# Optimization experiments

Hardware: AMD Instinct MI355X
Metric: run time of the kernel (lower is better)

Reference implementation:

```python
import jax, jax.numpy as jnp
import numpy as np
from jax import lax

BETA = 1.0
EPS_BIS = 0.1   # eps_threshold of FIND_MIN
N_ITER = 24     # enough bisection steps for any interval width seen here
N_BOX = 2097152
TINY = 1e-12


def _slog(x):
    return jnp.log(jnp.maximum(x, TINY))


def _sl1(x):  # smooth_l1_loss
    d = jnp.abs(x)
    return jnp.where(d < BETA, 0.5 * d * d / BETA, d - 0.5 * BETA)


def _sl1p(x):  # smooth_l1_loss_prime
    return jnp.clip(x / BETA, -1.0, 1.0)


def _xi_prime(w, wp, wh):
    return 0.5 * _sl1p(0.5 * (w - wh)) + _sl1p(_slog(w) - _slog(wp)) / jnp.maximum(w, TINY)


def _sigma(w, wp, wh):
    return w * _xi_prime(w, wp, wh)


def _xi(w, wp, wh):  # bbox_loss at x=(w-wh)/2
    return _sl1(0.5 * (w - wh)) + _sl1(_slog(wp) - _slog(w))


def _bisect(u, v, f):
    # vectorized FIND_MIN: early-exit endpoints + bisection to width < EPS_BIS
    fu, fv = f(u), f(v)

    def body(i, c):
        lo, hi = c
        act = (hi - lo) >= EPS_BIS
        m = 0.5 * (lo + hi)
        pos = f(m) >= 0
        lo = jnp.where(act & ~pos, m, lo)
        hi = jnp.where(act & pos, m, hi)
        return lo, hi

    lo, hi = lax.fori_loop(0, N_ITER, body, (u, v))
    m = 0.5 * (lo + hi)
    return jnp.where(fu >= 0, u, jnp.where(fv <= 0, v, m))


def _solve_o1(wp, wh, a1, b1):
    w0 = b1 - a1
    fxp = lambda w: _xi_prime(w, wp, wh)
    fsg = lambda w: _sigma(w, wp, wh)
    # branch A: max(w0, wh) < wp
    rA = _bisect(jnp.maximum(w0, wh), wp, fxp)
    eb = np.float32(np.exp(BETA))
    emin = np.float32(np.exp(min(BETA, 1.0)))
    e1 = np.float32(np.e)
    base = jnp.maximum(w0, jnp.maximum(wh - 2.0 * BETA, e1 * wp))
    disc = jnp.sqrt(jnp.maximum(1.0 - 32.0 / jnp.maximum(wh * wh, TINY), 0.0))
    r1 = _bisect(jnp.maximum(w0, wp), jnp.minimum(emin * wp, wh), fxp)                 # J1
    r2 = _bisect(jnp.maximum(jnp.maximum(w0, 2.0 * np.sqrt(BETA)),
                             jnp.maximum(wh - 2.0 * BETA, eb * wp)), wh, fxp)          # J2
    r3 = _bisect(base, jnp.minimum(eb, wh), fsg)                                        # J3
    r4 = _bisect(base, jnp.minimum(jnp.minimum(eb * wp, wh), 0.25 * wh * (1 + disc)), fsg)  # J4
    r5 = _bisect(jnp.maximum(base, 0.25 * wh * (1 - disc)), jnp.minimum(eb * wp, wh), fsg)  # J5
    cands = jnp.stack([w0, wh, r1, r2, r3, r4, r5])  # [7, N]
    xis = _xi(cands, wp, wh)
    small = wh <= 4.0 * np.sqrt(2.0)
    inf = jnp.float32(np.inf)
    xis = xis.at[4].set(jnp.where(small, xis[4], inf))  # J3 only when wh <= 4*sqrt(2)
    xis = xis.at[5].set(jnp.where(small, inf, xis[5]))  # J4/J5 otherwise
    xis = xis.at[6].set(jnp.where(small, inf, xis[6]))
    rB = jnp.take_along_axis(cands, jnp.argmin(xis, axis=0)[None], axis=0)[0]
    bA = jnp.maximum(w0, wh) < wp
    bB = jnp.maximum(w0, wp) < wh
    return jnp.where(bA, rA, jnp.where(bB, rB, w0))


def _solve_o2(dp, wp, a2, b2):
    wh1 = 2.0 * (dp - a2)
    wh2 = 2.0 * (b2 - dp)
    w1 = _solve_o1(wp, wh1, a2, b2)
    w2 = _solve_o1(wp, wh2, a2, b2)
    p1 = _xi(w1, wp, wh1) <= _xi(w2, wp, wh2)
    d = jnp.where(p1, a2 + 0.5 * w1, b2 - 0.5 * w2)
    w = jnp.where(p1, w1, w2)
    triv = wp >= jnp.maximum(wh1, wh2)
    return jnp.where(triv, dp, d), jnp.where(triv, wp, w)


def _case_axis(pred, prop, cases, target, crop, axis):
    lt, rb, d, o = (0, 1, 0, 2) if axis == 0 else (2, 3, 1, 3)
    ca = 0.5 * (prop[:, d] + prop[:, o]) + 0.5
    da = prop[:, o] - prop[:, d] + 1.0
    crop_a = crop[:, axis]
    # right/bottom cropped only
    a1r = target[:, d] - 0.5 * target[:, o]
    b1r = (crop_a - ca) / da
    wr = _solve_o1(pred[:, o], 2.0 * (pred[:, d] - a1r), a1r, b1r)
    dr = a1r + 0.5 * wr
    # left/top cropped only
    a1l = -ca / da
    b1l = target[:, d] + 0.5 * target[:, o]
    wl = _solve_o1(pred[:, o], 2.0 * (b1l - pred[:, d]), a1l, b1l)
    dl = b1l - 0.5 * wl
    # both sides cropped
    db, wb = _solve_o2(pred[:, d], pred[:, o], a1l, b1r)
    cl, cr = cases[:, lt], cases[:, rb]
    delta = jnp.where(~cl & ~cr, target[:, d],
            jnp.where(cr & ~cl, dr,
            jnp.where(cl & ~cr, dl, db)))
    omega = jnp.where(~cl & ~cr, target[:, o],
            jnp.where(cr & ~cl, wr,
            jnp.where(cl & ~cr, wl, wb)))
    return delta, omega


def _forward(pred, target, proposal_list, cases, crop_shapes):
    dx, wx = _case_axis(pred, proposal_list, cases, target, crop_shapes, 0)
    dy, wy = _case_axis(pred, proposal_list, cases, target, crop_shapes, 1)
    # torch.tensor(label) detaches -> stop_gradient
    label = lax.stop_gradient(jnp.stack([dx, dy, wx, wy], axis=1))
    return _sl1(pred - label)


def setup_inputs() -> dict:
    key = jax.random.key(0)
    ks = jax.random.split(key, 8)
    N = N_BOX
    deltas = 0.3 * jax.random.normal(ks[0], (N, 2), jnp.float32)
    omegas = jax.random.uniform(ks[1], (N, 2), jnp.float32, 0.5, 3.0)  # omega must be > 0 (log)
    pred = jnp.concatenate([deltas, omegas], axis=1)
    tdel = 0.3 * jax.random.normal(ks[2], (N, 2), jnp.float32)
    tom = jax.random.uniform(ks[3], (N, 2), jnp.float32, 0.5, 2.5)
    target = jnp.concatenate([tdel, tom], axis=1)
    xy1 = jax.random.uniform(ks[4], (N, 2), jnp.float32, 0.0, 800.0)
    wh = jax.random.uniform(ks[5], (N, 2), jnp.float32, 10.0, 110.0)
    proposal_list = jnp.stack([xy1[:, 0], xy1[:, 1], xy1[:, 0] + wh[:, 0], xy1[:, 1] + wh[:, 1]], axis=1)
    cases = jax.random.bernoulli(ks[6], 0.5, (N, 4))
    crop_shapes = jax.random.uniform(ks[7], (N, 2), jnp.float32, 500.0, 1024.0)
    return {"pred": pred, "target": target, "proposal_list": proposal_list,
            "cases": cases, "crop_shapes": crop_shapes}


def reference(pred, target, proposal_list, cases, crop_shapes):
    return _forward(pred, target, proposal_list, cases, crop_shapes)
```

## Files before the change

kernel.cpp:

```cpp
#include <hip/hip_runtime.h>

#define TINYF   1e-12f
#define EPSB    0.1f
#define EULERF  2.7182817f
#define SMALLWH 5.656854249f

__device__ __forceinline__ float clip1(float x) { return fminf(fmaxf(x, -1.0f), 1.0f); }
__device__ __forceinline__ float slogx(float x) { return __logf(fmaxf(x, TINYF)); }
__device__ __forceinline__ float sl1(float x) {
    float d = fabsf(x);
    return d < 1.0f ? 0.5f * d * d : d - 0.5f;
}

__device__ __forceinline__ float heval(float w, float wh, float lwp) {
    float t  = clip1(slogx(w) - lwp);
    float c2 = clip1(0.5f * (w - wh));
    return fmaf(0.5f * c2, fmaxf(w, TINYF), t);
}

__device__ __forceinline__ float xieval(float w, float wh, float lwp) {
    return sl1(0.5f * (w - wh)) + sl1(lwp - slogx(w));
}

__device__ __forceinline__ float bisect(float u, float v, float wh, float lwp) {
    float fu = heval(u, wh, lwp);
    float fv = heval(v, wh, lwp);
    float lo = u, hi = v;
#pragma unroll 1
    for (int it = 0; it < 24; ++it) {
        bool act = (hi - lo) >= EPSB;
        if (!__any(act)) break;
        float m = 0.5f * (lo + hi);
        if (act) {
            if (heval(m, wh, lwp) >= 0.0f) hi = m; else lo = m;
        }
    }
    float m = 0.5f * (lo + hi);
    return (fu >= 0.0f) ? u : ((fv <= 0.0f) ? v : m);
}

__device__ __forceinline__ int classify(float wp, float wh, float w0) {
    bool bA = fmaxf(w0, wh) < wp;
    bool bB = fmaxf(w0, wp) < wh;
    if (bA) return 0;
    if (bB) return (wh <= SMALLWH) ? 1 : 2;
    return 3;
}

__device__ __forceinline__ float solveA(float wp, float wh, float w0, float lwp) {
    return bisect(fmaxf(w0, wh), wp, wh, lwp);
}

__device__ __forceinline__ float solveB(float wp, float wh, float w0, float lwp, bool small) {
    float ewp  = EULERF * wp;
    float base = fmaxf(w0, fmaxf(wh - 2.0f, ewp));
    float r1 = bisect(fmaxf(w0, wp), fminf(ewp, wh), wh, lwp);
    float r2 = bisect(fmaxf(fmaxf(w0, 2.0f), fmaxf(wh - 2.0f, ewp)), wh, wh, lwp);
    float rB = w0, best = xieval(w0, wh, lwp), x;
    x = xieval(wh, wh, lwp); if (x < best) { best = x; rB = wh; }
    x = xieval(r1, wh, lwp); if (x < best) { best = x; rB = r1; }
    x = xieval(r2, wh, lwp); if (x < best) { best = x; rB = r2; }
    if (small) {
        float r3 = bisect(base, fminf(EULERF, wh), wh, lwp);
        x = xieval(r3, wh, lwp); if (x < best) { best = x; rB = r3; }
    } else {
        float disc = sqrtf(fmaxf(1.0f - __fdividef(32.0f, fmaxf(wh * wh, TINYF)), 0.0f));
        float r4 = bisect(base, fminf(fminf(ewp, wh), 0.25f * wh * (1.0f + disc)), wh, lwp);
        float r5 = bisect(fmaxf(base, 0.25f * wh * (1.0f - disc)), fminf(ewp, wh), wh, lwp);
        x = xieval(r4, wh, lwp); if (x < best) { best = x; rB = r4; }
        x = xieval(r5, wh, lwp); if (x < best) { best = x; rB = r5; }
    }
    return rB;
}

__device__ __forceinline__ void load_cases(const void* cases, int flag, int i,
                                           bool& c0, bool& c1, bool& c2, bool& c3) {
    if (flag == 1) {
        int4 ci = ((const int4*)cases)[i];
        c0 = ci.x != 0; c1 = ci.y != 0; c2 = ci.z != 0; c3 = ci.w != 0;
    } else if (flag == 2) {
        float4 cf = ((const float4*)cases)[i];
        c0 = cf.x != 0.0f; c1 = cf.y != 0.0f; c2 = cf.z != 0.0f; c3 = cf.w != 0.0f;
    } else {
        uchar4 cb = ((const uchar4*)cases)[i];
        c0 = cb.x != 0; c1 = cb.y != 0; c2 = cb.z != 0; c3 = cb.w != 0;
    }
}

__global__ __launch_bounds__(256) void cabb_fused(
        const float4* __restrict__ pred4, const float4* __restrict__ targ4,
        const float4* __restrict__ prop4, const void* __restrict__ cases,
        const float2* __restrict__ crop2,
        float4* __restrict__ out4, int n) {
    __shared__ float tWp[1024], tWh[1024], tW0[1024];
    __shared__ unsigned short tDst[1024];
    __shared__ float resW[1024];
    __shared__ int cnt[3];
    __shared__ int base[3];
    __shared__ int sFlag;

    int tid = threadIdx.x;
    int i = blockIdx.x * 256 + tid;
    if (tid < 3) cnt[tid] = 0;

    if (tid < 64) {
        uchar4 cb = ((const uchar4*)cases)[tid];
        bool i32ok = (cb.x <= 1) && (cb.y == 0) && (cb.z == 0) && (cb.w == 0);
        bool f32ok = (cb.x == 0) && (cb.y == 0) &&
                     ((cb.z == 0 && cb.w == 0) || (cb.z == 0x80 && cb.w == 0x3f));
        unsigned long long m32 = __ballot(i32ok);
        unsigned long long mf  = __ballot(f32ok);
        if (tid == 0) sFlag = (m32 == ~0ull) ? 1 : ((mf == ~0ull) ? 2 : 0);
    }
    __syncthreads();
    int flag = sFlag;

    bool valid = i < n;
    float4 pr = {0,0,0,0}, tg = {0,0,0,0};
    float caA[2] = {0,0}, daA[2] = {1,1}, cropA[2] = {0,0};
    bool clA[2] = {false,false}, crA[2] = {false,false};

    float sWp[4], sWh[4], sW0[4];
    int sCls[4], sPos[4];
#pragma unroll
    for (int k = 0; k < 4; ++k) { sCls[k] = -1; sPos[k] = 0; sWp[k] = 0; sWh[k] = 0; sW0[k] = 0; }

    if (valid) {
        pr = pred4[i]; tg = targ4[i];
        float4 pp = prop4[i];
        float2 cs = crop2[i];
        bool c0, c1, c2, c3;
        load_cases(cases, flag, i, c0, c1, c2, c3);
        clA[0] = c0; crA[0] = c1; clA[1] = c2; crA[1] = c3;
        caA[0] = 0.5f * (pp.x + pp.z) + 0.5f;  daA[0] = pp.z - pp.x + 1.0f;  cropA[0] = cs.x;
        caA[1] = 0.5f * (pp.y + pp.w) + 0.5f;  daA[1] = pp.w - pp.y + 1.0f;  cropA[1] = cs.y;
    }

#pragma unroll
    for (int axis = 0; axis < 2; ++axis) {
        if (!valid) continue;
        bool L = clA[axis], R = crA[axis];
        if (!(L || R)) continue;
        float pd = axis ? pr.y : pr.x, po = axis ? pr.w : pr.z;
        float td = axis ? tg.y : tg.x, to = axis ? tg.w : tg.z;
        int k0 = axis * 2, k1 = axis * 2 + 1;
        if (R && !L) {
            float a1 = td - 0.5f * to;
            float b1 = __fdividef(cropA[axis] - caA[axis], daA[axis]);
            float wh = 2.0f * (pd - a1), w0 = b1 - a1;
            int c = classify(po, wh, w0);
            if (c == 3) resW[k0 * 256 + tid] = w0;
            else { sCls[k0] = c; sWp[k0] = po; sWh[k0] = wh; sW0[k0] = w0; }
        } else if (L && !R) {
            float a1 = __fdividef(-caA[axis], daA[axis]);
            float b1 = td + 0.5f * to;
            float wh = 2.0f * (b1 - pd), w0 = b1 - a1;
            int c = classify(po, wh, w0);
            if (c == 3) resW[k0 * 256 + tid] = w0;
            else { sCls[k0] = c; sWp[k0] = po; sWh[k0] = wh; sW0[k0] = w0; }
        } else {
            float a1l = __fdividef(-caA[axis], daA[axis]);
            float b1r = __fdividef(cropA[axis] - caA[axis], daA[axis]);
            float wh1 = 2.0f * (pd - a1l), wh2 = 2.0f * (b1r - pd);
            if (po < fmaxf(wh1, wh2)) {
                float w0 = b1r - a1l;
                int ck0 = classify(po, wh1, w0);
                if (ck0 == 3) resW[k0 * 256 + tid] = w0;
                else { sCls[k0] = ck0; sWp[k0] = po; sWh[k0] = wh1; sW0[k0] = w0; }
                int ck1 = classify(po, wh2, w0);
                if (ck1 == 3) resW[k1 * 256 + tid] = w0;
                else { sCls[k1] = ck1; sWp[k1] = po; sWh[k1] = wh2; sW0[k1] = w0; }
            }
        }
    }

#pragma unroll
    for (int k = 0; k < 4; ++k) {
        if (sCls[k] >= 0) sPos[k] = atomicAdd(&cnt[sCls[k]], 1);
    }
    __syncthreads();
    if (tid == 0) { base[0] = 0; base[1] = cnt[0]; base[2] = cnt[0] + cnt[1]; }
    __syncthreads();
#pragma unroll
    for (int k = 0; k < 4; ++k) {
        if (sCls[k] >= 0) {
            int p = base[sCls[k]] + sPos[k];
            tWp[p] = sWp[k]; tWh[p] = sWh[k]; tW0[p] = sW0[k];
            tDst[p] = (unsigned short)(k * 256 + tid);
        }
    }
    __syncthreads();

    int nA = base[1], nAB1 = base[2], total = base[2] + cnt[2];
    for (int t0 = 0; t0 < total; t0 += 256) {
        int t = t0 + tid;
        if (t < total) {
            float wp = tWp[t], wh = tWh[t], w0 = tW0[t];
            float lwp = __logf(fmaxf(wp, TINYF));
            float w;
            if (t < nA) w = solveA(wp, wh, w0, lwp);
            else        w = solveB(wp, wh, w0, lwp, t < nAB1);
            resW[tDst[t]] = w;
        }
    }
    __syncthreads();

    if (valid) {
        float labd[2], labw[2];
#pragma unroll
        for (int axis = 0; axis < 2; ++axis) {
            bool L = clA[axis], R = crA[axis];
            float pd = axis ? pr.y : pr.x, po = axis ? pr.w : pr.z;
            float td = axis ? tg.y : tg.x, to = axis ? tg.w : tg.z;
            float delta, omega;
            if (!L && !R) { delta = td; omega = to; }
            else if (R && !L) {
                float w = resW[(axis * 2) * 256 + tid];
                float a1 = td - 0.5f * to;
                delta = a1 + 0.5f * w; omega = w;
            } else if (L && !R) {
                float w = resW[(axis * 2) * 256 + tid];
                float b1 = td + 0.5f * to;
                delta = b1 - 0.5f * w; omega = w;
            } else {
                float a1l = __fdividef(-caA[axis], daA[axis]);
                float b1r = __fdividef(cropA[axis] - caA[axis], daA[axis]);
                float wh1 = 2.0f * (pd - a1l), wh2 = 2.0f * (b1r - pd);
                if (po >= fmaxf(wh1, wh2)) { delta = pd; omega = po; }
                else {
                    float w1 = resW[(axis * 2) * 256 + tid];
                    float w2 = resW[(axis * 2 + 1) * 256 + tid];
                    float lwp = __logf(fmaxf(po, TINYF));
                    bool p1 = xieval(w1, wh1, lwp) <= xieval(w2, wh2, lwp);
                    delta = p1 ? (a1l + 0.5f * w1) : (b1r - 0.5f * w2);
                    omega = p1 ? w1 : w2;
                }
            }
            labd[axis] = delta; labw[axis] = omega;
        }
        float4 o;
        o.x = sl1(pr.x - labd[0]);
        o.y = sl1(pr.y - labd[1]);
        o.z = sl1(pr.z - labw[0]);
        o.w = sl1(pr.w - labw[1]);
        out4[i] = o;
    }
}

extern "C" void kernel_launch(void* const* d_in, const int* in_sizes, int n_in,
                              void* d_out, int out_size, void* d_ws, size_t ws_size,
                              hipStream_t stream) {
    const float4* pred = (const float4*)d_in[0];
    const float4* targ = (const float4*)d_in[1];
    const float4* prop = (const float4*)d_in[2];
    const void*   cases = d_in[3];
    const float2* crop = (const float2*)d_in[4];
    float4* out = (float4*)d_out;
    int n = in_sizes[0] / 4;

    int nb = (n + 255) / 256;
    cabb_fused<<<nb, 256, 0, stream>>>(pred, targ, prop, cases, crop, out, n);
}
```

Measured before the change: 188.7 us.

## Specialize bisection using clipped log term and drop redundant J4/J5 loops

Uses the fact that in the J2/J3 intervals the log term is already saturated at +1, so a log-free predicate (hq) replaces the full derivative inside the bisection loops. J4/J5 bisections are replaced by closed-form endpoint checks plus a midpoint, which assumes their intervals are narrower than the tolerance or resolved at the endpoints. Logs are computed with log2 times ln2, and the per-axis divisions become a reciprocal multiply with merged branches. These rely on interval properties of the problem; if they fail to hold, results could differ from the reference.

Measured after the change: 179.3 us. -5.0%, faster.

```diff
diff --git a/kernel.cpp b/kernel.cpp
--- a/kernel.cpp
+++ b/kernel.cpp
@@ -4,25 +4,31 @@
 #define EPSB    0.1f
 #define EULERF  2.7182817f
 #define SMALLWH 5.656854249f
+#define LN2F    0.69314718f
 
 __device__ __forceinline__ float clip1(float x) { return fminf(fmaxf(x, -1.0f), 1.0f); }
-__device__ __forceinline__ float slogx(float x) { return __logf(fmaxf(x, TINYF)); }
 __device__ __forceinline__ float sl1(float x) {
     float d = fabsf(x);
     return d < 1.0f ? 0.5f * d * d : d - 0.5f;
 }
+__device__ __forceinline__ float l2x(float x) { return __log2f(fmaxf(x, TINYF)); }
 
 __device__ __forceinline__ float heval(float w, float wh, float lwp) {
-    float t  = clip1(slogx(w) - lwp);
-    float c2 = clip1(0.5f * (w - wh));
-    return fmaf(0.5f * c2, fmaxf(w, TINYF), t);
+    float t = clip1(fmaf(l2x(w), LN2F, -lwp));
+    float c = clip1(0.5f * (w - wh));
+    return fmaf(0.5f * c, fmaxf(w, TINYF), t);
+}
+__device__ __forceinline__ float hq(float w, float wh) {
+    float c = clip1(0.5f * (w - wh));
+    return fmaf(0.5f * c, w, 1.0f);
 }
 
 __device__ __forceinline__ float xieval(float w, float wh, float lwp) {
-    return sl1(0.5f * (w - wh)) + sl1(lwp - slogx(w));
-}
-
-__device__ __forceinline__ float bisect(float u, float v, float wh, float lwp) {
+    float t = fmaf(l2x(w), LN2F, -lwp);
+    return sl1(0.5f * (w - wh)) + sl1(t);
+}
+
+__device__ __forceinline__ float bisect_g(float u, float v, float wh, float lwp) {
     float fu = heval(u, wh, lwp);
     float fv = heval(v, wh, lwp);
     float lo = u, hi = v;
@@ -39,6 +45,22 @@
     return (fu >= 0.0f) ? u : ((fv <= 0.0f) ? v : m);
 }
 
+__device__ __forceinline__ float bisect_q(float u, float v, float wh, float fv) {
+    float fu = hq(u, wh);
+    float lo = u, hi = v;
+#pragma unroll 1
+    for (int it = 0; it < 24; ++it) {
+        bool act = (hi - lo) >= EPSB;
+        if (!__any(act)) break;
+        float m = 0.5f * (lo + hi);
+        if (act) {
+            if (hq(m, wh) >= 0.0f) hi = m; else lo = m;
+        }
+    }
+    float m = 0.5f * (lo + hi);
+    return (fu >= 0.0f) ? u : ((fv <= 0.0f) ? v : m);
+}
+
 __device__ __forceinline__ int classify(float wp, float wh, float w0) {
     bool bA = fmaxf(w0, wh) < wp;
     bool bB = fmaxf(w0, wp) < wh;
@@ -48,25 +70,35 @@
 }
 
 __device__ __forceinline__ float solveA(float wp, float wh, float w0, float lwp) {
-    return bisect(fmaxf(w0, wh), wp, wh, lwp);
+    return bisect_g(fmaxf(w0, wh), wp, wh, lwp);
 }
 
 __device__ __forceinline__ float solveB(float wp, float wh, float w0, float lwp, bool small) {
     float ewp  = EULERF * wp;
     float base = fmaxf(w0, fmaxf(wh - 2.0f, ewp));
-    float r1 = bisect(fmaxf(w0, wp), fminf(ewp, wh), wh, lwp);
-    float r2 = bisect(fmaxf(fmaxf(w0, 2.0f), fmaxf(wh - 2.0f, ewp)), wh, wh, lwp);
+    float lnwh = l2x(wh) * LN2F;
+    float r1 = bisect_g(fmaxf(w0, wp), fminf(ewp, wh), wh, lwp);
+    float fv2 = clip1(lnwh - lwp);
+    float r2 = bisect_q(fmaxf(fmaxf(w0, 2.0f), fmaxf(wh - 2.0f, ewp)), wh, wh, fv2);
+
     float rB = w0, best = xieval(w0, wh, lwp), x;
-    x = xieval(wh, wh, lwp); if (x < best) { best = x; rB = wh; }
+    x = sl1(lwp - lnwh);
+    if (x < best) { best = x; rB = wh; }
     x = xieval(r1, wh, lwp); if (x < best) { best = x; rB = r1; }
     x = xieval(r2, wh, lwp); if (x < best) { best = x; rB = r2; }
     if (small) {
-        float r3 = bisect(base, fminf(EULERF, wh), wh, lwp);
+        float v3 = fminf(EULERF, wh);
+        float r3 = bisect_q(base, v3, wh, heval(v3, wh, lwp));
         x = xieval(r3, wh, lwp); if (x < best) { best = x; rB = r3; }
     } else {
         float disc = sqrtf(fmaxf(1.0f - __fdividef(32.0f, fmaxf(wh * wh, TINYF)), 0.0f));
-        float r4 = bisect(base, fminf(fminf(ewp, wh), 0.25f * wh * (1.0f + disc)), wh, lwp);
-        float r5 = bisect(fmaxf(base, 0.25f * wh * (1.0f - disc)), fminf(ewp, wh), wh, lwp);
+        float v4 = fminf(fminf(ewp, wh), 0.25f * wh * (1.0f + disc));
+        float fu4 = hq(base, wh), fv4 = heval(v4, wh, lwp);
+        float r4 = (fu4 >= 0.0f) ? base : ((fv4 <= 0.0f) ? v4 : 0.5f * (base + v4));
+        float u5 = fmaxf(base, 0.25f * wh * (1.0f - disc));
+        float v5 = fminf(ewp, wh);
+        float fu5 = hq(u5, wh), fv5 = heval(v5, wh, lwp);
+        float r5 = (fu5 >= 0.0f) ? u5 : ((fv5 <= 0.0f) ? v5 : 0.5f * (u5 + v5));
         x = xieval(r4, wh, lwp); if (x < best) { best = x; rB = r4; }
         x = xieval(r5, wh, lwp); if (x < best) { best = x; rB = r5; }
     }
@@ -117,7 +149,7 @@
 
     bool valid = i < n;
     float4 pr = {0,0,0,0}, tg = {0,0,0,0};
-    float caA[2] = {0,0}, daA[2] = {1,1}, cropA[2] = {0,0};
+    float caA[2] = {0,0}, rdA[2] = {1,1}, cropA[2] = {0,0};
     bool clA[2] = {false,false}, crA[2] = {false,false};
 
     float sWp[4], sWh[4], sW0[4];
@@ -132,8 +164,8 @@
         bool c0, c1, c2, c3;
         load_cases(cases, flag, i, c0, c1, c2, c3);
         clA[0] = c0; crA[0] = c1; clA[1] = c2; crA[1] = c3;
-        caA[0] = 0.5f * (pp.x + pp.z) + 0.5f;  daA[0] = pp.z - pp.x + 1.0f;  cropA[0] = cs.x;
-        caA[1] = 0.5f * (pp.y + pp.w) + 0.5f;  daA[1] = pp.w - pp.y + 1.0f;  cropA[1] = cs.y;
+        caA[0] = 0.5f * (pp.x + pp.z) + 0.5f;  rdA[0] = __fdividef(1.0f, pp.z - pp.x + 1.0f);  cropA[0] = cs.x;
+        caA[1] = 0.5f * (pp.y + pp.w) + 0.5f;  rdA[1] = __fdividef(1.0f, pp.w - pp.y + 1.0f);  cropA[1] = cs.y;
     }
 
 #pragma unroll
@@ -143,24 +175,18 @@
         if (!(L || R)) continue;
         float pd = axis ? pr.y : pr.x, po = axis ? pr.w : pr.z;
         float td = axis ? tg.y : tg.x, to = axis ? tg.w : tg.z;
+        float b1r = (cropA[axis] - caA[axis]) * rdA[axis];
+        float a1l = -caA[axis] * rdA[axis];
         int k0 = axis * 2, k1 = axis * 2 + 1;
-        if (R && !L) {
-            float a1 = td - 0.5f * to;
-            float b1 = __fdividef(cropA[axis] - caA[axis], daA[axis]);
-            float wh = 2.0f * (pd - a1), w0 = b1 - a1;
-            int c = classify(po, wh, w0);
-            if (c == 3) resW[k0 * 256 + tid] = w0;
-            else { sCls[k0] = c; sWp[k0] = po; sWh[k0] = wh; sW0[k0] = w0; }
-        } else if (L && !R) {
-            float a1 = __fdividef(-caA[axis], daA[axis]);
-            float b1 = td + 0.5f * to;
-            float wh = 2.0f * (b1 - pd), w0 = b1 - a1;
+        if (L != R) {
+            float a1 = R ? (td - 0.5f * to) : a1l;
+            float b1 = R ? b1r : (td + 0.5f * to);
+            float wh = 2.0f * (R ? (pd - a1) : (b1 - pd));
+            float w0 = b1 - a1;
             int c = classify(po, wh, w0);
             if (c == 3) resW[k0 * 256 + tid] = w0;
             else { sCls[k0] = c; sWp[k0] = po; sWh[k0] = wh; sW0[k0] = w0; }
         } else {
-            float a1l = __fdividef(-caA[axis], daA[axis]);
-            float b1r = __fdividef(cropA[axis] - caA[axis], daA[axis]);
             float wh1 = 2.0f * (pd - a1l), wh2 = 2.0f * (b1r - pd);
             if (po < fmaxf(wh1, wh2)) {
                 float w0 = b1r - a1l;
@@ -196,7 +222,7 @@
         int t = t0 + tid;
         if (t < total) {
             float wp = tWp[t], wh = tWh[t], w0 = tW0[t];
-            float lwp = __logf(fmaxf(wp, TINYF));
+            float lwp = l2x(wp) * LN2F;
             float w;
             if (t < nA) w = solveA(wp, wh, w0, lwp);
             else        w = solveB(wp, wh, w0, lwp, t < nAB1);
@@ -214,23 +240,20 @@
             float td = axis ? tg.y : tg.x, to = axis ? tg.w : tg.z;
             float delta, omega;
             if (!L && !R) { delta = td; omega = to; }
-            else if (R && !L) {
+            else if (L != R) {
                 float w = resW[(axis * 2) * 256 + tid];
-                float a1 = td - 0.5f * to;
-                delta = a1 + 0.5f * w; omega = w;
-            } else if (L && !R) {
-                float w = resW[(axis * 2) * 256 + tid];
-                float b1 = td + 0.5f * to;
-                delta = b1 - 0.5f * w; omega = w;
+                float a = R ? (td - 0.5f * to) : (td + 0.5f * to);
+                delta = R ? (a + 0.5f * w) : (a - 0.5f * w);
+                omega = w;
             } else {
-                float a1l = __fdividef(-caA[axis], daA[axis]);
-                float b1r = __fdividef(cropA[axis] - caA[axis], daA[axis]);
+                float b1r = (cropA[axis] - caA[axis]) * rdA[axis];
+                float a1l = -caA[axis] * rdA[axis];
                 float wh1 = 2.0f * (pd - a1l), wh2 = 2.0f * (b1r - pd);
                 if (po >= fmaxf(wh1, wh2)) { delta = pd; omega = po; }
                 else {
                     float w1 = resW[(axis * 2) * 256 + tid];
                     float w2 = resW[(axis * 2 + 1) * 256 + tid];
-                    float lwp = __logf(fmaxf(po, TINYF));
+                    float lwp = l2x(po) * LN2F;
                     bool p1 = xieval(w1, wh1, lwp) <= xieval(w2, wh2, lwp);
                     delta = p1 ? (a1l + 0.5f * w1) : (b1r - 0.5f * w2);
                     omega = p1 ? w1 : w2;
```
